# Kernel tuning notes

Hardware: AMD Instinct MI355X
Metric: run time of the kernel (lower is better)

Reference implementation:

```python
import jax, jax.numpy as jnp
import numpy as np

B, S, D_IN, D_K, D_OUT = 8, 2048, 1024, 64, 64

def setup_inputs() -> dict:
    key = jax.random.key(0)
    k1, k2, k3, k4 = jax.random.split(key, 4)
    sc = 1.0 / np.sqrt(D_IN)
    return {
        "X": jax.random.normal(k1, (B, S, D_IN), dtype=jnp.float32),
        "Wq": jax.random.normal(k2, (D_IN, D_K), dtype=jnp.float32) * sc,
        "Wk": jax.random.normal(k3, (D_IN, D_K), dtype=jnp.float32) * sc,
        "Wv": jax.random.normal(k4, (D_IN, D_OUT), dtype=jnp.float32) * sc,
    }

def reference(X, Wq, Wk, Wv):
    # projections (no bias)
    Q = jnp.einsum('bsd,dk->bsk', X, Wq)   # [B,S,d_k]
    K = jnp.einsum('bsd,dk->bsk', X, Wk)   # [B,S,d_k]
    V = jnp.einsum('bsd,dv->bsv', X, Wv)   # [B,S,d_out]
    d_k = Q.shape[-1]
    S_mat = jnp.einsum('bqk,bsk->bqs', Q, K) / jnp.sqrt(jnp.float32(d_k))
    # causal mask: positions j > i get -inf
    causal = jnp.tril(jnp.ones((X.shape[1], X.shape[1]), dtype=bool))
    S_mat = jnp.where(causal[None, :, :], S_mat, -jnp.inf)
    A = jax.nn.softmax(S_mat, axis=-1)
    return jnp.einsum('bqs,bsv->bqv', A, V)
```

## Files before the change

kernel.cpp:

```cpp
#include <hip/hip_runtime.h>
#include <hip/hip_bf16.h>
#include <cstdint>
#include <cstddef>

#define BATCH 8
#define SEQ   2048
#define DIN   1024

typedef float f32x4 __attribute__((ext_vector_type(4)));
typedef float f32x8 __attribute__((ext_vector_type(8)));
typedef __bf16 bf16x8 __attribute__((ext_vector_type(8)));
typedef unsigned short ushort8_t __attribute__((ext_vector_type(8)));

__device__ __forceinline__ unsigned short bfu(float f) {
  __bf16 h = (__bf16)f;
  return __builtin_bit_cast(unsigned short, h);
}

__device__ __forceinline__ bf16x8 cvt8pair(float4 a, float4 b) {
  f32x8 v;
  v[0] = a.x; v[1] = a.y; v[2] = a.z; v[3] = a.w;
  v[4] = b.x; v[5] = b.y; v[6] = b.z; v[7] = b.w;
  return __builtin_convertvector(v, bf16x8);
}

__global__ void pack_w(const float* __restrict__ Wq, const float* __restrict__ Wk,
                       const float* __restrict__ Wv, unsigned short* __restrict__ Wp) {
  const int t = blockIdx.x * blockDim.x + threadIdx.x;
  const int lane = t & 63;
  const int grp = t >> 6;
  const int ks = grp & 31;
  const int nt = grp >> 5;
  const int n = nt * 16 + (lane & 15);
  const int k0 = ks * 32 + ((lane >> 4) << 3);
  const float* W;
  int col;
  float scale = 1.0f;
  if (n < 64)       { W = Wq; col = n;       scale = 0.125f; }
  else if (n < 128) { W = Wk; col = n - 64;  }
  else              { W = Wv; col = n - 128; }
  ushort8_t out;
#pragma unroll
  for (int j = 0; j < 8; ++j)
    out[j] = bfu(W[(size_t)(k0 + j) * 64 + col] * scale);
  reinterpret_cast<ushort8_t*>(Wp)[t] = out;
}

__global__ __launch_bounds__(256, 1) void qkv_gemm(
    const float* __restrict__ X, const unsigned short* __restrict__ Wp,
    unsigned short* __restrict__ Qb, unsigned short* __restrict__ Kb,
    unsigned short* __restrict__ Vt) {
  const int lane = threadIdx.x & 63;
  const int wave = threadIdx.x >> 6;
  const int l15 = lane & 15;
  const int quad = lane >> 4;
  const int m0 = blockIdx.x * 64;
  const int nt0 = wave * 3;

  const float* xbase = X + (size_t)(m0 + l15) * DIN + quad * 8;
  const ushort8_t* wp = reinterpret_cast<const ushort8_t*>(Wp) + (size_t)nt0 * 2048 + lane;

  f32x4 acc[4][3];
#pragma unroll
  for (int mt = 0; mt < 4; ++mt)
#pragma unroll
    for (int nt = 0; nt < 3; ++nt) acc[mt][nt] = (f32x4){0.f, 0.f, 0.f, 0.f};

  float4 na[4][2];
#pragma unroll
  for (int mt = 0; mt < 4; ++mt) {
    const float* p = xbase + (size_t)(mt * 16) * DIN;
    na[mt][0] = reinterpret_cast<const float4*>(p)[0];
    na[mt][1] = reinterpret_cast<const float4*>(p)[1];
  }

  for (int ks = 0; ks < 32; ++ks) {
    bf16x8 a[4];
#pragma unroll
    for (int mt = 0; mt < 4; ++mt) a[mt] = cvt8pair(na[mt][0], na[mt][1]);
    if (ks < 31) {
#pragma unroll
      for (int mt = 0; mt < 4; ++mt) {
        const float* p = xbase + (size_t)(mt * 16) * DIN + (ks + 1) * 32;
        na[mt][0] = reinterpret_cast<const float4*>(p)[0];
        na[mt][1] = reinterpret_cast<const float4*>(p)[1];
      }
    }
    const ushort8_t* wk = wp + ks * 64;
#pragma unroll
    for (int nt = 0; nt < 3; ++nt) {
      bf16x8 bfm = __builtin_bit_cast(bf16x8, wk[(size_t)nt * 2048]);
#pragma unroll
      for (int mt = 0; mt < 4; ++mt)
        acc[mt][nt] = __builtin_amdgcn_mfma_f32_16x16x32_bf16(a[mt], bfm, acc[mt][nt], 0, 0, 0);
    }
  }

#pragma unroll
  for (int mt = 0; mt < 4; ++mt) {
    const int srow = m0 + mt * 16 + quad * 4;
    const int b = srow >> 11;
    const int s = srow & 2047;
#pragma unroll
    for (int nt = 0; nt < 3; ++nt) {
      const int n = (nt0 + nt) * 16 + l15;
      if (n < 64) {
#pragma unroll
        for (int r = 0; r < 4; ++r)
          Qb[(size_t)(srow + r) * 64 + n] = bfu(acc[mt][nt][r]);
      } else if (n < 128) {
#pragma unroll
        for (int r = 0; r < 4; ++r)
          Kb[(size_t)(srow + r) * 64 + (n - 64)] = bfu(acc[mt][nt][r]);
      } else {
        const int dv = n - 128;
        ushort4 t4;
        t4.x = bfu(acc[mt][nt][0]); t4.y = bfu(acc[mt][nt][1]);
        t4.z = bfu(acc[mt][nt][2]); t4.w = bfu(acc[mt][nt][3]);
        *reinterpret_cast<ushort4*>(Vt + (((size_t)(b * 64 + dv)) << 11) + s) = t4;
      }
    }
  }
}

__global__ __launch_bounds__(256, 2) void flash_kernel(
    const unsigned short* __restrict__ Qb, const unsigned short* __restrict__ Kb,
    const unsigned short* __restrict__ Vt, float* __restrict__ Out) {
  __shared__ float Olds[4][2][16][68];
  __shared__ float Llds[4][2][16];
  __shared__ unsigned short Pf[4][2][2][64 * 8];

  const int tid = threadIdx.x;
  const int lane = tid & 63;
  const int wave = tid >> 6;
  const int l15 = lane & 15;
  const int quad = lane >> 4;

  const int g = blockIdx.x;
  const int batch = g & 7;
  const int qb = 63 - (g >> 3);
  const int q0 = qb * 32;
  const int n64 = (q0 + 95) >> 6;

  bf16x8 qf[2][2];
#pragma unroll
  for (int mt = 0; mt < 2; ++mt) {
    const ushort8_t* qp = reinterpret_cast<const ushort8_t*>(
        Qb + (size_t)(batch * SEQ + q0 + mt * 16 + l15) * 64);
    qf[mt][0] = __builtin_bit_cast(bf16x8, qp[quad]);
    qf[mt][1] = __builtin_bit_cast(bf16x8, qp[4 + quad]);
  }

  f32x4 o[2][4];
  float lacc[2][4];
#pragma unroll
  for (int mt = 0; mt < 2; ++mt)
#pragma unroll
    for (int i = 0; i < 4; ++i) {
      o[mt][i] = (f32x4){0.f, 0.f, 0.f, 0.f};
      lacc[mt][i] = 0.f;
    }

  for (int kt = wave; kt < n64; kt += 4) {
    const int k0 = kt * 64;
    f32x4 s[2][4];
#pragma unroll
    for (int h = 0; h < 4; ++h) {
      const ushort8_t* kp = reinterpret_cast<const ushort8_t*>(
          Kb + (size_t)(batch * SEQ + k0 + h * 16 + l15) * 64);
      bf16x8 kf0 = __builtin_bit_cast(bf16x8, kp[quad]);
      bf16x8 kf1 = __builtin_bit_cast(bf16x8, kp[4 + quad]);
#pragma unroll
      for (int mt = 0; mt < 2; ++mt) {
        f32x4 z = (f32x4){0.f, 0.f, 0.f, 0.f};
        z = __builtin_amdgcn_mfma_f32_16x16x32_bf16(qf[mt][0], kf0, z, 0, 0, 0);
        z = __builtin_amdgcn_mfma_f32_16x16x32_bf16(qf[mt][1], kf1, z, 0, 0, 0);
        s[mt][h] = z;
      }
    }
    if (kt == n64 - 1) {
#pragma unroll
      for (int mt = 0; mt < 2; ++mt)
#pragma unroll
        for (int h = 0; h < 4; ++h) {
          const int col = k0 + h * 16 + l15;
#pragma unroll
          for (int r = 0; r < 4; ++r) {
            const int row = q0 + mt * 16 + quad * 4 + r;
            if (col > row) s[mt][h][r] = -INFINITY;
          }
        }
    }
#pragma unroll
    for (int mt = 0; mt < 2; ++mt) {
#pragma unroll
      for (int h = 0; h < 4; ++h) {
        const int c = h >> 1;
        const int lp = ((h & 1) * 2 + (l15 >> 3)) * 16 + quad * 4;
        const int j = l15 & 7;
#pragma unroll
        for (int r = 0; r < 4; ++r) {
          const float pv = __expf(s[mt][h][r]);
          lacc[mt][r] += pv;
          Pf[wave][mt][c][(lp + r) * 8 + j] = bfu(pv);
        }
      }
    }
#pragma unroll
    for (int c = 0; c < 2; ++c) {
      bf16x8 pfm[2];
#pragma unroll
      for (int mt = 0; mt < 2; ++mt)
        pfm[mt] = __builtin_bit_cast(bf16x8,
            reinterpret_cast<const ushort8_t*>(&Pf[wave][mt][c][0])[lane]);
#pragma unroll
      for (int nt = 0; nt < 4; ++nt) {
        const ushort8_t* vp = reinterpret_cast<const ushort8_t*>(
            Vt + (((size_t)(batch * 64 + nt * 16 + l15)) << 11) + k0 + c * 32);
        bf16x8 vf = __builtin_bit_cast(bf16x8, vp[quad]);
#pragma unroll
        for (int mt = 0; mt < 2; ++mt)
          o[mt][nt] = __builtin_amdgcn_mfma_f32_16x16x32_bf16(pfm[mt], vf, o[mt][nt], 0, 0, 0);
      }
    }
  }

#pragma unroll
  for (int off = 1; off < 16; off <<= 1)
#pragma unroll
    for (int mt = 0; mt < 2; ++mt)
#pragma unroll
      for (int r = 0; r < 4; ++r)
        lacc[mt][r] += __shfl_xor(lacc[mt][r], off, 64);

#pragma unroll
  for (int mt = 0; mt < 2; ++mt) {
#pragma unroll
    for (int nt = 0; nt < 4; ++nt)
#pragma unroll
      for (int r = 0; r < 4; ++r)
        Olds[wave][mt][quad * 4 + r][nt * 16 + l15] = o[mt][nt][r];
    if (l15 == 0) {
#pragma unroll
      for (int r = 0; r < 4; ++r) Llds[wave][mt][quad * 4 + r] = lacc[mt][r];
    }
  }
  __syncthreads();

  const int col = tid & 63;
  const int r0 = tid >> 6;
#pragma unroll
  for (int row = r0; row < 32; row += 4) {
    const int mt = row >> 4;
    const int rr = row & 15;
    float lstar = 0.f, accv = 0.f;
#pragma unroll
    for (int w = 0; w < 4; ++w) {
      lstar += Llds[w][mt][rr];
      accv += Olds[w][mt][rr][col];
    }
    Out[(size_t)(batch * SEQ + q0 + row) * 64 + col] = accv / lstar;
  }
}

extern "C" void kernel_launch(void* const* d_in, const int* in_sizes, int n_in,
                              void* d_out, int out_size, void* d_ws, size_t ws_size,
                              hipStream_t stream) {
  const float* X  = (const float*)d_in[0];
  const float* Wq = (const float*)d_in[1];
  const float* Wk = (const float*)d_in[2];
  const float* Wv = (const float*)d_in[3];
  float* Out = (float*)d_out;

  char* ws = (char*)d_ws;
  unsigned short* Wp = (unsigned short*)ws;
  unsigned short* Qb = (unsigned short*)(ws + (400 << 10));
  unsigned short* Kb = (unsigned short*)(ws + (400 << 10) + (2 << 20));
  unsigned short* Vt = (unsigned short*)(ws + (400 << 10) + (4 << 20));

  pack_w<<<96, 256, 0, stream>>>(Wq, Wk, Wv, Wp);
  qkv_gemm<<<256, 256, 0, stream>>>(X, Wp, Qb, Kb, Vt);
  flash_kernel<<<512, 256, 0, stream>>>(Qb, Kb, Vt, Out);
}
```

Baseline: 149.9 us.

## Stage X tile through double-buffered LDS and prefetch weights in QKV GEMM

In the QKV projection GEMM, each wave used to load and convert the full 64-row X tile to bf16 by itself. Now the block loads X cooperatively once per k-step, converts it, and writes it into a double-buffered shared-memory tile that all four waves read. Weight fragments are prefetched two steps ahead into registers. This removes the four-fold redundant global X reads and conversions, at the cost of a __syncthreads per k-step and added LDS traffic. Launch-bound minimum-occupancy hints are also dropped from both kernels.

Measured after the change: 155.2 us. 3.6% more time.

```diff
diff --git a/kernel.cpp b/kernel.cpp
--- a/kernel.cpp
+++ b/kernel.cpp
@@ -46,54 +46,73 @@
   reinterpret_cast<ushort8_t*>(Wp)[t] = out;
 }
 
-__global__ __launch_bounds__(256, 1) void qkv_gemm(
+__global__ __launch_bounds__(256) void qkv_gemm(
     const float* __restrict__ X, const unsigned short* __restrict__ Wp,
     unsigned short* __restrict__ Qb, unsigned short* __restrict__ Kb,
     unsigned short* __restrict__ Vt) {
-  const int lane = threadIdx.x & 63;
-  const int wave = threadIdx.x >> 6;
+  __shared__ unsigned short Ab[2][64 * 40];
+
+  const int tid = threadIdx.x;
+  const int lane = tid & 63;
+  const int wave = tid >> 6;
   const int l15 = lane & 15;
   const int quad = lane >> 4;
   const int m0 = blockIdx.x * 64;
   const int nt0 = wave * 3;
 
-  const float* xbase = X + (size_t)(m0 + l15) * DIN + quad * 8;
+  const int st_r = tid >> 2;
+  const int st_c = tid & 3;
+  const float* xs = X + (size_t)(m0 + st_r) * DIN + st_c * 8;
+  unsigned short* const aw = &Ab[0][0] + st_r * 40 + st_c * 8;
   const ushort8_t* wp = reinterpret_cast<const ushort8_t*>(Wp) + (size_t)nt0 * 2048 + lane;
 
-  f32x4 acc[4][3];
-#pragma unroll
-  for (int mt = 0; mt < 4; ++mt)
-#pragma unroll
-    for (int nt = 0; nt < 3; ++nt) acc[mt][nt] = (f32x4){0.f, 0.f, 0.f, 0.f};
-
-  float4 na[4][2];
-#pragma unroll
-  for (int mt = 0; mt < 4; ++mt) {
-    const float* p = xbase + (size_t)(mt * 16) * DIN;
-    na[mt][0] = reinterpret_cast<const float4*>(p)[0];
-    na[mt][1] = reinterpret_cast<const float4*>(p)[1];
-  }
+  f32x4 acc[12];
+#pragma unroll
+  for (int i = 0; i < 12; ++i) acc[i] = (f32x4){0.f, 0.f, 0.f, 0.f};
+
+  float4 xa = reinterpret_cast<const float4*>(xs)[0];
+  float4 xb2 = reinterpret_cast<const float4*>(xs)[1];
+  *reinterpret_cast<ushort8_t*>(aw) =
+      __builtin_bit_cast(ushort8_t, cvt8pair(xa, xb2));
+  xa = reinterpret_cast<const float4*>(xs + 32)[0];
+  xb2 = reinterpret_cast<const float4*>(xs + 32)[1];
+  ushort8_t breg[2][3];
+#pragma unroll
+  for (int p = 0; p < 2; ++p)
+#pragma unroll
+    for (int nt = 0; nt < 3; ++nt) breg[p][nt] = wp[p * 64 + (size_t)nt * 2048];
+  __syncthreads();
 
   for (int ks = 0; ks < 32; ++ks) {
-    bf16x8 a[4];
-#pragma unroll
-    for (int mt = 0; mt < 4; ++mt) a[mt] = cvt8pair(na[mt][0], na[mt][1]);
-    if (ks < 31) {
-#pragma unroll
-      for (int mt = 0; mt < 4; ++mt) {
-        const float* p = xbase + (size_t)(mt * 16) * DIN + (ks + 1) * 32;
-        na[mt][0] = reinterpret_cast<const float4*>(p)[0];
-        na[mt][1] = reinterpret_cast<const float4*>(p)[1];
-      }
-    }
-    const ushort8_t* wk = wp + ks * 64;
-#pragma unroll
-    for (int nt = 0; nt < 3; ++nt) {
-      bf16x8 bfm = __builtin_bit_cast(bf16x8, wk[(size_t)nt * 2048]);
-#pragma unroll
-      for (int mt = 0; mt < 4; ++mt)
-        acc[mt][nt] = __builtin_amdgcn_mfma_f32_16x16x32_bf16(a[mt], bfm, acc[mt][nt], 0, 0, 0);
-    }
+    const int p = ks & 1;
+    if (ks < 31)
+      *reinterpret_cast<ushort8_t*>(aw + ((ks + 1) & 1) * (64 * 40)) =
+          __builtin_bit_cast(ushort8_t, cvt8pair(xa, xb2));
+    if (ks < 30) {
+      xa = reinterpret_cast<const float4*>(xs + (ks + 2) * 32)[0];
+      xb2 = reinterpret_cast<const float4*>(xs + (ks + 2) * 32)[1];
+    }
+    bf16x8 af[4];
+#pragma unroll
+    for (int mt = 0; mt < 4; ++mt)
+      af[mt] = __builtin_bit_cast(bf16x8,
+          *reinterpret_cast<const ushort8_t*>(
+              &Ab[p][(mt * 16 + l15) * 40 + quad * 8]));
+    bf16x8 b0 = __builtin_bit_cast(bf16x8, breg[p][0]);
+    bf16x8 b1 = __builtin_bit_cast(bf16x8, breg[p][1]);
+    bf16x8 b2 = __builtin_bit_cast(bf16x8, breg[p][2]);
+    if (ks < 30) {
+#pragma unroll
+      for (int nt = 0; nt < 3; ++nt)
+        breg[p][nt] = wp[(ks + 2) * 64 + (size_t)nt * 2048];
+    }
+#pragma unroll
+    for (int mt = 0; mt < 4; ++mt) {
+      acc[mt * 3 + 0] = __builtin_amdgcn_mfma_f32_16x16x32_bf16(af[mt], b0, acc[mt * 3 + 0], 0, 0, 0);
+      acc[mt * 3 + 1] = __builtin_amdgcn_mfma_f32_16x16x32_bf16(af[mt], b1, acc[mt * 3 + 1], 0, 0, 0);
+      acc[mt * 3 + 2] = __builtin_amdgcn_mfma_f32_16x16x32_bf16(af[mt], b2, acc[mt * 3 + 2], 0, 0, 0);
+    }
+    __syncthreads();
   }
 
 #pragma unroll
@@ -103,27 +122,28 @@
     const int s = srow & 2047;
 #pragma unroll
     for (int nt = 0; nt < 3; ++nt) {
+      const f32x4 a = acc[mt * 3 + nt];
       const int n = (nt0 + nt) * 16 + l15;
       if (n < 64) {
 #pragma unroll
         for (int r = 0; r < 4; ++r)
-          Qb[(size_t)(srow + r) * 64 + n] = bfu(acc[mt][nt][r]);
+          Qb[(size_t)(srow + r) * 64 + n] = bfu(a[r]);
       } else if (n < 128) {
 #pragma unroll
         for (int r = 0; r < 4; ++r)
-          Kb[(size_t)(srow + r) * 64 + (n - 64)] = bfu(acc[mt][nt][r]);
+          Kb[(size_t)(srow + r) * 64 + (n - 64)] = bfu(a[r]);
       } else {
         const int dv = n - 128;
         ushort4 t4;
-        t4.x = bfu(acc[mt][nt][0]); t4.y = bfu(acc[mt][nt][1]);
-        t4.z = bfu(acc[mt][nt][2]); t4.w = bfu(acc[mt][nt][3]);
+        t4.x = bfu(a[0]); t4.y = bfu(a[1]);
+        t4.z = bfu(a[2]); t4.w = bfu(a[3]);
         *reinterpret_cast<ushort4*>(Vt + (((size_t)(b * 64 + dv)) << 11) + s) = t4;
       }
     }
   }
 }
 
-__global__ __launch_bounds__(256, 2) void flash_kernel(
+__global__ __launch_bounds__(256) void flash_kernel(
     const unsigned short* __restrict__ Qb, const unsigned short* __restrict__ Kb,
     const unsigned short* __restrict__ Vt, float* __restrict__ Out) {
   __shared__ float Olds[4][2][16][68];
```
